# Kernel tuning notes

Hardware: AMD Instinct MI355X
Metric: run time of the kernel (lower is better)

The kernel has to match this reference:

```python
import jax, jax.numpy as jnp
import numpy as np

N_NODES = 80000
N_EDGES = 1280000
D_NODE = 128
D_EDGE = 32
D_HID = 64
NEG_SLOPE = 0.2


def setup_inputs() -> dict:
    key = jax.random.key(0)
    ks = jax.random.split(key, 9)
    return {
        "node_features": jax.random.normal(ks[0], (N_NODES, D_NODE), dtype=jnp.float32),
        "edge_features": jax.random.normal(ks[1], (N_EDGES, D_EDGE), dtype=jnp.float32),
        "edge_index": jax.random.randint(ks[2], (2, N_EDGES), 0, N_NODES, dtype=jnp.int64),
        # params: w (node Linear), edgew (edge Linear), attn (3*hid -> 1)
        "w_w": jax.random.normal(ks[3], (D_NODE, D_HID), dtype=jnp.float32) / np.sqrt(D_NODE),
        "w_b": jax.random.normal(ks[4], (D_HID,), dtype=jnp.float32) * 0.01,
        "ew_w": jax.random.normal(ks[5], (D_EDGE, D_HID), dtype=jnp.float32) / np.sqrt(D_EDGE),
        "ew_b": jax.random.normal(ks[6], (D_HID,), dtype=jnp.float32) * 0.01,
        "a_w": jax.random.normal(ks[7], (3 * D_HID, 1), dtype=jnp.float32) / np.sqrt(3 * D_HID),
        "a_b": jax.random.normal(ks[8], (1,), dtype=jnp.float32) * 0.01,
    }


def reference(node_features, edge_features, edge_index, w_w, w_b, ew_w, ew_b, a_w, a_b):
    n_nodes = node_features.shape[0]
    h = node_features @ w_w + w_b              # [N, H]
    edge_h = edge_features @ ew_w + ew_b       # [E, H]
    tgt = edge_index[0]                        # target (softmax group) nodes i
    nbr = edge_index[1]                        # neighbor nodes j
    h_i = h[tgt]                               # [E, H] gather
    h_j = h[nbr]                               # [E, H] gather
    h_concat = jnp.concatenate([h_i, h_j, edge_h], axis=-1)  # [E, 3H]
    eij = jax.nn.leaky_relu(h_concat @ a_w + a_b, negative_slope=NEG_SLOPE)  # [E, 1]
    # scatter-softmax over edges grouped by target node (numerically stable)
    seg_max = jax.ops.segment_max(eij, tgt, num_segments=n_nodes)            # [N, 1]
    ex = jnp.exp(eij - seg_max[tgt])
    seg_sum = jax.ops.segment_sum(ex, tgt, num_segments=n_nodes)             # [N, 1]
    alpha = ex / seg_sum[tgt]                                                # [E, 1]
    # (dropout omitted for deterministic reference)
    message = alpha * h_j                                                    # [E, H]
    out = jax.ops.segment_sum(message, tgt, num_segments=n_nodes)            # [N, H]
    return jax.nn.elu(out)
```

## Files before the change

kernel.cpp:

```cpp
#include <hip/hip_runtime.h>
#include <math.h>

#define N_NODES 80000
#define N_EDGES 1280000
#define D_NODE  128
#define D_EDGE  32
#define D_HID   64
#define NEG_SLOPE 0.2f
#define NB 313
#define CAP 4608
#define BCNT_STRIDE 16
#define EB_BLK 512
#define EB_CHUNK 2048
#define EB_NCHUNK (N_EDGES / EB_CHUNK)

__device__ inline float waveReduceSum(float v) {
    #pragma unroll
    for (int o = 32; o > 0; o >>= 1) v += __shfl_xor(v, o);
    return v;
}
__device__ inline unsigned short f2bf(float f) {
    unsigned u = __float_as_uint(f);
    return (unsigned short)((u + 0x7FFF + ((u >> 16) & 1)) >> 16);
}
__device__ inline float bf2f(unsigned short v) {
    return __uint_as_float(((unsigned)v) << 16);
}

__global__ __launch_bounds__(256) void node_kernel(
        const float* __restrict__ nf, const float* __restrict__ w_w,
        const float* __restrict__ w_b, const float* __restrict__ a_w,
        unsigned short* __restrict__ hb, float* __restrict__ s1, float* __restrict__ s2) {
    __shared__ float Ws[D_HID * D_NODE];
    __shared__ float Xs[32][D_NODE];
    for (int i = threadIdx.x; i < D_NODE * D_HID; i += 256) {
        int k = i >> 6, d = i & 63;
        Ws[d * D_NODE + (((k >> 2) ^ (d & 7)) << 2) + (k & 3)] = w_w[i];
    }
    int lane = threadIdx.x & 63;
    int wv   = threadIdx.x >> 6;
    float wb = w_b[lane];
    float a1 = a_w[lane];
    float a2 = a_w[D_HID + lane];
    const float* wrow = &Ws[lane * D_NODE];
    const int nTiles = N_NODES / 32;
    for (int tile = blockIdx.x; tile < nTiles; tile += gridDim.x) {
        int n0 = tile * 32;
        __syncthreads();
        {
            const float4* src = (const float4*)(nf + (size_t)n0 * D_NODE);
            float4* dst = (float4*)&Xs[0][0];
            #pragma unroll
            for (int j = 0; j < 4; ++j)
                dst[threadIdx.x + 256 * j] = src[threadIdx.x + 256 * j];
        }
        __syncthreads();
        float acc[8] = {0.f, 0.f, 0.f, 0.f, 0.f, 0.f, 0.f, 0.f};
        const float* xs = &Xs[wv * 8][0];
        #pragma unroll 4
        for (int k4 = 0; k4 < 32; ++k4) {
            float4 w = *(const float4*)&wrow[(k4 ^ (lane & 7)) << 2];
            #pragma unroll
            for (int n = 0; n < 8; ++n) {
                float4 x = *(const float4*)&xs[n * D_NODE + (k4 << 2)];
                acc[n] += w.x * x.x + w.y * x.y + w.z * x.z + w.w * x.w;
            }
        }
        #pragma unroll
        for (int n = 0; n < 8; ++n) {
            int node = n0 + wv * 8 + n;
            float hv = acc[n] + wb;
            hb[(size_t)node * D_HID + lane] = f2bf(hv);
            float r1 = waveReduceSum(hv * a1);
            float r2 = waveReduceSum(hv * a2);
            if (lane == 0) { s1[node] = r1; s2[node] = r2; }
        }
    }
}

__global__ __launch_bounds__(EB_BLK) void edge_bin_kernel(
        const float* __restrict__ ef, const int* __restrict__ eidx,
        const float* __restrict__ s2v,
        const float* __restrict__ ew_w, const float* __restrict__ ew_b,
        const float* __restrict__ a_w, const float* __restrict__ a_b,
        int* __restrict__ bcnt, int2* __restrict__ binned) {
    __shared__ float cs[D_EDGE];
    __shared__ float bes;
    __shared__ int hist[NB], gbase[NB], rank[NB];
    __shared__ int scanbuf[512];
    __shared__ float sq [EB_CHUNK];
    __shared__ int2  sval[EB_CHUNK];
    __shared__ int   sdst[EB_CHUNK];
    int tid = threadIdx.x;
    if (tid < D_EDGE) {
        float s = 0.f;
        #pragma unroll
        for (int d = 0; d < D_HID; ++d) s += ew_w[tid * D_HID + d] * a_w[2 * D_HID + d];
        cs[tid] = s;
    } else if (tid == D_EDGE) {
        float s = 0.f;
        #pragma unroll
        for (int d = 0; d < D_HID; ++d) s += ew_b[d] * a_w[2 * D_HID + d];
        bes = s + a_b[0];
    }
    int qd = tid >> 2;
    int j  = tid & 3;
    for (int c = blockIdx.x; c < EB_NCHUNK; c += gridDim.x) {
        for (int i = tid; i < NB; i += EB_BLK) { hist[i] = 0; rank[i] = 0; }
        __syncthreads();
        int e0 = c * EB_CHUNK;
        int RT[4], RN[4];
        #pragma unroll
        for (int k = 0; k < 4; ++k) {
            int idx = k * EB_BLK + tid;
            int e = e0 + idx;
            RT[k] = eidx[e];
            RN[k] = eidx[N_EDGES + e];
            sq[idx] = bes + s2v[RN[k]];
            atomicAdd(&hist[RT[k] >> 8], 1);
        }
        __syncthreads();
        #pragma unroll 2
        for (int rr = 0; rr < EB_CHUNK / 128; ++rr) {
            int idx = rr * 128 + qd;
            int e = e0 + idx;
            const float4* f4 = (const float4*)ef;
            float4 fa = f4[(size_t)e * 8 + j];
            float4 fb = f4[(size_t)e * 8 + 4 + j];
            const float4 c1 = *(const float4*)&cs[j * 4];
            const float4 c2 = *(const float4*)&cs[16 + j * 4];
            float p = fa.x * c1.x + fa.y * c1.y + fa.z * c1.z + fa.w * c1.w
                    + fb.x * c2.x + fb.y * c2.y + fb.z * c2.z + fb.w * c2.w;
            p += __shfl_xor(p, 1);
            p += __shfl_xor(p, 2);
            if (j == 0) sq[idx] += p;
        }
        __syncthreads();
        for (int i = tid; i < NB; i += EB_BLK) {
            int cc = hist[i];
            if (cc) gbase[i] = i * CAP + atomicAdd(&bcnt[i * BCNT_STRIDE], cc);
        }
        scanbuf[tid] = (tid < NB) ? hist[tid] : 0;
        __syncthreads();
        for (int ofs = 1; ofs < 512; ofs <<= 1) {
            int t = (tid >= (unsigned)ofs) ? scanbuf[tid - ofs] : 0;
            __syncthreads();
            scanbuf[tid] += t;
            __syncthreads();
        }
        #pragma unroll
        for (int k = 0; k < 4; ++k) {
            int idx = k * EB_BLK + tid;
            int tg = RT[k];
            int b  = tg >> 8;
            int r  = atomicAdd(&rank[b], 1);
            int slot = scanbuf[b] - hist[b] + r;
            sval[slot] = make_int2(((tg & 255) << 17) | RN[k],
                                   __float_as_int(sq[idx]));
            sdst[slot] = gbase[b] + r;
        }
        __syncthreads();
        #pragma unroll
        for (int k = 0; k < 4; ++k) {
            int i = k * EB_BLK + tid;
            binned[sdst[i]] = sval[i];
        }
        __syncthreads();
    }
}

__global__ __launch_bounds__(1024) void bucket_accum_kernel(
        const int* __restrict__ bcnt, const int2* __restrict__ binned,
        const float* __restrict__ s1, const unsigned short* __restrict__ hb,
        float* __restrict__ out) {
    __shared__ int nhist[256], buf[256], sbase[256], ncur[256];
    __shared__ int2 slab[CAP];
    int tid = threadIdx.x;
    int b = blockIdx.x;
    int in0 = b * CAP;
    int cnt = bcnt[b * BCNT_STRIDE];
    if (tid < 256) nhist[tid] = 0;
    __syncthreads();
    for (int i = tid; i < cnt; i += 1024)
        atomicAdd(&nhist[binned[in0 + i].x >> 17], 1);
    __syncthreads();
    if (tid < 256) buf[tid] = nhist[tid];
    __syncthreads();
    for (int ofs = 1; ofs < 256; ofs <<= 1) {
        int t = 0;
        if (tid < 256 && tid >= ofs) t = buf[tid - ofs];
        __syncthreads();
        if (tid < 256) buf[tid] += t;
        __syncthreads();
    }
    if (tid < 256) {
        int excl = buf[tid] - nhist[tid];
        sbase[tid] = excl;
        ncur[tid]  = excl;
    }
    __syncthreads();
    for (int i = tid; i < cnt; i += 1024) {
        int2 p = binned[in0 + i];
        int r = atomicAdd(&ncur[p.x >> 17], 1);
        slab[r] = make_int2(p.x & 0x1FFFF, p.y);
    }
    __syncthreads();
    int grp = tid >> 4;
    int li  = tid & 15;
    int wl  = ((tid & 63) >> 4) << 4;
    for (int nl = grp; nl < 256; nl += 64) {
        int node = b * 256 + nl;
        if (node >= N_NODES) break;
        int base = sbase[nl];
        int cn   = nhist[nl];
        float s1i = s1[node];
        float ax = 0.f, ay = 0.f, az = 0.f, aw = 0.f, sumex = 0.f;
        for (int c0 = 0; c0 < cn; c0 += 16) {
            int i = c0 + li;
            int nc = min(16, cn - c0);
            float exv = 0.f; int nbv = 0;
            if (i < cn) {
                int2 p = slab[base + i];
                nbv = p.x;
                float s = s1i + __int_as_float(p.y);
                s = (s > 0.f) ? s : NEG_SLOPE * s;
                exv = __expf(s);
            }
            sumex += exv;
            for (int jj = 0; jj < nc; ++jj) {
                float w  = __shfl(exv, wl + jj);
                int   nb = __shfl(nbv, wl + jj);
                uint2 v = *(const uint2*)&hb[(size_t)nb * D_HID + li * 4];
                ax += w * bf2f((unsigned short)(v.x & 0xFFFF));
                ay += w * bf2f((unsigned short)(v.x >> 16));
                az += w * bf2f((unsigned short)(v.y & 0xFFFF));
                aw += w * bf2f((unsigned short)(v.y >> 16));
            }
        }
        #pragma unroll
        for (int o = 8; o > 0; o >>= 1) sumex += __shfl_xor(sumex, o);
        float4 o4;
        if (cn == 0) {
            o4 = make_float4(0.f, 0.f, 0.f, 0.f);
        } else {
            o4.x = ax / sumex; o4.y = ay / sumex; o4.z = az / sumex; o4.w = aw / sumex;
            o4.x = (o4.x > 0.f) ? o4.x : (__expf(o4.x) - 1.f);
            o4.y = (o4.y > 0.f) ? o4.y : (__expf(o4.y) - 1.f);
            o4.z = (o4.z > 0.f) ? o4.z : (__expf(o4.z) - 1.f);
            o4.w = (o4.w > 0.f) ? o4.w : (__expf(o4.w) - 1.f);
        }
        ((float4*)out)[(size_t)node * 16 + li] = o4;
    }
}

extern "C" void kernel_launch(void* const* d_in, const int* in_sizes, int n_in,
                              void* d_out, int out_size, void* d_ws, size_t ws_size,
                              hipStream_t stream) {
    const float* nf   = (const float*)d_in[0];
    const float* ef   = (const float*)d_in[1];
    const int*   eidx = (const int*)d_in[2];
    const float* w_w  = (const float*)d_in[3];
    const float* w_b  = (const float*)d_in[4];
    const float* ew_w = (const float*)d_in[5];
    const float* ew_b = (const float*)d_in[6];
    const float* a_w  = (const float*)d_in[7];
    const float* a_b  = (const float*)d_in[8];
    float* out = (float*)d_out;

    char* ws = (char*)d_ws;
    size_t o = 0;
    auto alloc = [&](size_t bytes) -> void* {
        void* p = ws + o;
        o = (o + bytes + 255) & ~(size_t)255;
        return p;
    };
    unsigned short* hb  = (unsigned short*)alloc((size_t)N_NODES * D_HID * 2);
    float* s1       = (float*)alloc((size_t)N_NODES * 4);
    float* s2       = (float*)alloc((size_t)N_NODES * 4);
    int*   bcnt     = (int*)alloc((size_t)NB * BCNT_STRIDE * 4);
    int2*  binned   = (int2*)alloc((size_t)NB * CAP * 8);

    hipMemsetAsync(bcnt, 0, (size_t)NB * BCNT_STRIDE * 4, stream);

    node_kernel<<<1250, 256, 0, stream>>>(nf, w_w, w_b, a_w, hb, s1, s2);
    edge_bin_kernel<<<EB_NCHUNK, EB_BLK, 0, stream>>>(ef, eidx, s2, ew_w, ew_b, a_w, a_b, bcnt, binned);
    bucket_accum_kernel<<<NB, 1024, 0, stream>>>(bcnt, binned, s1, hb, out);
}
```

Measured before the change: 147.2 us.

## Fuse node projection and edge binning into one kernel; defer s2 gather

Merges the node linear kernel and the edge binning kernel into a single launch whose blocks are split by index into edge-binning blocks and node-projection blocks, so the two independent phases run concurrently. To remove the dependency of binning on the node scores, the per-neighbor s2 term is no longer gathered during binning and is instead gathered in the accumulation kernel. This trades one extra random gather per edge in the final kernel for overlap of the two phases and one fewer kernel launch. Node blocks now use 512 threads with 4 nodes per wave.

```diff
diff --git a/kernel.cpp b/kernel.cpp
--- a/kernel.cpp
+++ b/kernel.cpp
@@ -10,9 +10,10 @@
 #define NB 313
 #define CAP 4608
 #define BCNT_STRIDE 16
-#define EB_BLK 512
 #define EB_CHUNK 2048
-#define EB_NCHUNK (N_EDGES / EB_CHUNK)
+#define EB_NBLK 625
+#define ND_NBLK 1250
+#define ND_TILES 2500
 
 __device__ inline float waveReduceSum(float v) {
     #pragma unroll
@@ -27,116 +28,69 @@
     return __uint_as_float(((unsigned)v) << 16);
 }
 
-__global__ __launch_bounds__(256) void node_kernel(
-        const float* __restrict__ nf, const float* __restrict__ w_w,
-        const float* __restrict__ w_b, const float* __restrict__ a_w,
-        unsigned short* __restrict__ hb, float* __restrict__ s1, float* __restrict__ s2) {
-    __shared__ float Ws[D_HID * D_NODE];
-    __shared__ float Xs[32][D_NODE];
-    for (int i = threadIdx.x; i < D_NODE * D_HID; i += 256) {
-        int k = i >> 6, d = i & 63;
-        Ws[d * D_NODE + (((k >> 2) ^ (d & 7)) << 2) + (k & 3)] = w_w[i];
-    }
-    int lane = threadIdx.x & 63;
-    int wv   = threadIdx.x >> 6;
-    float wb = w_b[lane];
-    float a1 = a_w[lane];
-    float a2 = a_w[D_HID + lane];
-    const float* wrow = &Ws[lane * D_NODE];
-    const int nTiles = N_NODES / 32;
-    for (int tile = blockIdx.x; tile < nTiles; tile += gridDim.x) {
-        int n0 = tile * 32;
-        __syncthreads();
-        {
-            const float4* src = (const float4*)(nf + (size_t)n0 * D_NODE);
-            float4* dst = (float4*)&Xs[0][0];
-            #pragma unroll
-            for (int j = 0; j < 4; ++j)
-                dst[threadIdx.x + 256 * j] = src[threadIdx.x + 256 * j];
-        }
-        __syncthreads();
-        float acc[8] = {0.f, 0.f, 0.f, 0.f, 0.f, 0.f, 0.f, 0.f};
-        const float* xs = &Xs[wv * 8][0];
-        #pragma unroll 4
-        for (int k4 = 0; k4 < 32; ++k4) {
-            float4 w = *(const float4*)&wrow[(k4 ^ (lane & 7)) << 2];
-            #pragma unroll
-            for (int n = 0; n < 8; ++n) {
-                float4 x = *(const float4*)&xs[n * D_NODE + (k4 << 2)];
-                acc[n] += w.x * x.x + w.y * x.y + w.z * x.z + w.w * x.w;
-            }
-        }
-        #pragma unroll
-        for (int n = 0; n < 8; ++n) {
-            int node = n0 + wv * 8 + n;
-            float hv = acc[n] + wb;
-            hb[(size_t)node * D_HID + lane] = f2bf(hv);
-            float r1 = waveReduceSum(hv * a1);
-            float r2 = waveReduceSum(hv * a2);
-            if (lane == 0) { s1[node] = r1; s2[node] = r2; }
-        }
-    }
-}
-
-__global__ __launch_bounds__(EB_BLK) void edge_bin_kernel(
-        const float* __restrict__ ef, const int* __restrict__ eidx,
-        const float* __restrict__ s2v,
+__global__ __launch_bounds__(512) void fused_kernel(
+        const float* __restrict__ nf, const float* __restrict__ ef,
+        const int* __restrict__ eidx,
+        const float* __restrict__ w_w, const float* __restrict__ w_b,
         const float* __restrict__ ew_w, const float* __restrict__ ew_b,
         const float* __restrict__ a_w, const float* __restrict__ a_b,
+        unsigned short* __restrict__ hb, float* __restrict__ s1, float* __restrict__ s2,
         int* __restrict__ bcnt, int2* __restrict__ binned) {
-    __shared__ float cs[D_EDGE];
-    __shared__ float bes;
-    __shared__ int hist[NB], gbase[NB], rank[NB];
-    __shared__ int scanbuf[512];
-    __shared__ float sq [EB_CHUNK];
-    __shared__ int2  sval[EB_CHUNK];
-    __shared__ int   sdst[EB_CHUNK];
+    __shared__ __align__(16) char smem[49152];
     int tid = threadIdx.x;
-    if (tid < D_EDGE) {
-        float s = 0.f;
-        #pragma unroll
-        for (int d = 0; d < D_HID; ++d) s += ew_w[tid * D_HID + d] * a_w[2 * D_HID + d];
-        cs[tid] = s;
-    } else if (tid == D_EDGE) {
-        float s = 0.f;
-        #pragma unroll
-        for (int d = 0; d < D_HID; ++d) s += ew_b[d] * a_w[2 * D_HID + d];
-        bes = s + a_b[0];
-    }
-    int qd = tid >> 2;
-    int j  = tid & 3;
-    for (int c = blockIdx.x; c < EB_NCHUNK; c += gridDim.x) {
-        for (int i = tid; i < NB; i += EB_BLK) { hist[i] = 0; rank[i] = 0; }
-        __syncthreads();
-        int e0 = c * EB_CHUNK;
+
+    if (blockIdx.x < EB_NBLK) {
+        float* cs      = (float*)smem;
+        float* besp    = (float*)(smem + 128);
+        int*   hist    = (int*)(smem + 256);
+        int*   gbase   = (int*)(smem + 1536);
+        int*   rank    = (int*)(smem + 2816);
+        int*   scanbuf = (int*)(smem + 4096);
+        float* sq      = (float*)(smem + 6144);
+        int2*  sval    = (int2*)(smem + 14336);
+        int*   sdst    = (int*)(smem + 30720);
+        if (tid < D_EDGE) {
+            float s = 0.f;
+            #pragma unroll
+            for (int d = 0; d < D_HID; ++d) s += ew_w[tid * D_HID + d] * a_w[2 * D_HID + d];
+            cs[tid] = s;
+        } else if (tid == D_EDGE) {
+            float s = 0.f;
+            #pragma unroll
+            for (int d = 0; d < D_HID; ++d) s += ew_b[d] * a_w[2 * D_HID + d];
+            *besp = s + a_b[0];
+        }
+        for (int i = tid; i < NB; i += 512) { hist[i] = 0; rank[i] = 0; }
+        __syncthreads();
+        float bes = *besp;
+        int e0 = blockIdx.x * EB_CHUNK;
         int RT[4], RN[4];
         #pragma unroll
         for (int k = 0; k < 4; ++k) {
-            int idx = k * EB_BLK + tid;
+            int idx = k * 512 + tid;
             int e = e0 + idx;
             RT[k] = eidx[e];
             RN[k] = eidx[N_EDGES + e];
-            sq[idx] = bes + s2v[RN[k]];
             atomicAdd(&hist[RT[k] >> 8], 1);
         }
-        __syncthreads();
+        int qd = tid >> 2, j = tid & 3;
+        const float4 c1 = *(const float4*)&cs[j * 4];
+        const float4 c2 = *(const float4*)&cs[16 + j * 4];
+        const float4* f4 = (const float4*)ef;
         #pragma unroll 2
         for (int rr = 0; rr < EB_CHUNK / 128; ++rr) {
             int idx = rr * 128 + qd;
             int e = e0 + idx;
-            const float4* f4 = (const float4*)ef;
             float4 fa = f4[(size_t)e * 8 + j];
             float4 fb = f4[(size_t)e * 8 + 4 + j];
-            const float4 c1 = *(const float4*)&cs[j * 4];
-            const float4 c2 = *(const float4*)&cs[16 + j * 4];
             float p = fa.x * c1.x + fa.y * c1.y + fa.z * c1.z + fa.w * c1.w
                     + fb.x * c2.x + fb.y * c2.y + fb.z * c2.z + fb.w * c2.w;
             p += __shfl_xor(p, 1);
             p += __shfl_xor(p, 2);
-            if (j == 0) sq[idx] += p;
-        }
-        __syncthreads();
-        for (int i = tid; i < NB; i += EB_BLK) {
+            if (j == 0) sq[idx] = p + bes;
+        }
+        __syncthreads();
+        for (int i = tid; i < NB; i += 512) {
             int cc = hist[i];
             if (cc) gbase[i] = i * CAP + atomicAdd(&bcnt[i * BCNT_STRIDE], cc);
         }
@@ -150,7 +104,7 @@
         }
         #pragma unroll
         for (int k = 0; k < 4; ++k) {
-            int idx = k * EB_BLK + tid;
+            int idx = k * 512 + tid;
             int tg = RT[k];
             int b  = tg >> 8;
             int r  = atomicAdd(&rank[b], 1);
@@ -162,17 +116,60 @@
         __syncthreads();
         #pragma unroll
         for (int k = 0; k < 4; ++k) {
-            int i = k * EB_BLK + tid;
+            int i = k * 512 + tid;
             binned[sdst[i]] = sval[i];
         }
-        __syncthreads();
+    } else {
+        float* Ws = (float*)smem;
+        float* Xs = (float*)(smem + 32768);
+        for (int i = tid; i < D_NODE * D_HID; i += 512) {
+            int k = i >> 6, d = i & 63;
+            Ws[d * D_NODE + (((k >> 2) ^ (d & 7)) << 2) + (k & 3)] = w_w[i];
+        }
+        int lane = tid & 63;
+        int wv   = tid >> 6;
+        float wb = w_b[lane];
+        float a1 = a_w[lane];
+        float a2 = a_w[D_HID + lane];
+        const float* wrow = &Ws[lane * D_NODE];
+        for (int tile = (int)blockIdx.x - EB_NBLK; tile < ND_TILES; tile += ND_NBLK) {
+            int n0 = tile * 32;
+            __syncthreads();
+            {
+                const float4* src = (const float4*)(nf + (size_t)n0 * D_NODE);
+                float4* dst = (float4*)Xs;
+                dst[tid]       = src[tid];
+                dst[tid + 512] = src[tid + 512];
+            }
+            __syncthreads();
+            float acc[4] = {0.f, 0.f, 0.f, 0.f};
+            const float* xs = &Xs[(size_t)wv * 4 * D_NODE];
+            #pragma unroll 4
+            for (int k4 = 0; k4 < 32; ++k4) {
+                float4 w = *(const float4*)&wrow[(k4 ^ (lane & 7)) << 2];
+                #pragma unroll
+                for (int n = 0; n < 4; ++n) {
+                    float4 x = *(const float4*)&xs[n * D_NODE + (k4 << 2)];
+                    acc[n] += w.x * x.x + w.y * x.y + w.z * x.z + w.w * x.w;
+                }
+            }
+            #pragma unroll
+            for (int n = 0; n < 4; ++n) {
+                int node = n0 + wv * 4 + n;
+                float hv = acc[n] + wb;
+                hb[(size_t)node * D_HID + lane] = f2bf(hv);
+                float r1 = waveReduceSum(hv * a1);
+                float r2 = waveReduceSum(hv * a2);
+                if (lane == 0) { s1[node] = r1; s2[node] = r2; }
+            }
+        }
     }
 }
 
 __global__ __launch_bounds__(1024) void bucket_accum_kernel(
         const int* __restrict__ bcnt, const int2* __restrict__ binned,
-        const float* __restrict__ s1, const unsigned short* __restrict__ hb,
-        float* __restrict__ out) {
+        const float* __restrict__ s1, const float* __restrict__ s2v,
+        const unsigned short* __restrict__ hb, float* __restrict__ out) {
     __shared__ int nhist[256], buf[256], sbase[256], ncur[256];
     __shared__ int2 slab[CAP];
     int tid = threadIdx.x;
@@ -222,7 +219,7 @@
             if (i < cn) {
                 int2 p = slab[base + i];
                 nbv = p.x;
-                float s = s1i + __int_as_float(p.y);
+                float s = s1i + __int_as_float(p.y) + s2v[nbv];
                 s = (s > 0.f) ? s : NEG_SLOPE * s;
                 exv = __expf(s);
             }
@@ -282,7 +279,7 @@
 
     hipMemsetAsync(bcnt, 0, (size_t)NB * BCNT_STRIDE * 4, stream);
 
-    node_kernel<<<1250, 256, 0, stream>>>(nf, w_w, w_b, a_w, hb, s1, s2);
-    edge_bin_kernel<<<EB_NCHUNK, EB_BLK, 0, stream>>>(ef, eidx, s2, ew_w, ew_b, a_w, a_b, bcnt, binned);
-    bucket_accum_kernel<<<NB, 1024, 0, stream>>>(bcnt, binned, s1, hb, out);
-}
+    fused_kernel<<<EB_NBLK + ND_NBLK, 512, 0, stream>>>(
+        nf, ef, eidx, w_w, w_b, ew_w, ew_b, a_w, a_b, hb, s1, s2, bcnt, binned);
+    bucket_accum_kernel<<<NB, 1024, 0, stream>>>(bcnt, binned, s1, s2, hb, out);
+}
```

Result: no change. 147.8 us (+0.4%).

## Move s2 gather into accumulate kernel and batch edge-feature loads for MLP

Applied to the files above, without the earlier changes.

Drops the per-edge random gather of s2[nbr] from the binning kernel and instead adds s2 inside the bucket accumulate kernel, where the neighbor index is already at hand. The edge-feature dot product now issues eight float4 loads per half before computing, to raise memory-level parallelism. The grid-stride loop is removed since the grid equals the chunk count. This decouples the binning kernel from the node kernel's s2 output, at the cost of an extra scattered 4-byte load per edge in the accumulate phase.

```diff
diff --git a/kernel.cpp b/kernel.cpp
--- a/kernel.cpp
+++ b/kernel.cpp
@@ -80,12 +80,11 @@
 
 __global__ __launch_bounds__(EB_BLK) void edge_bin_kernel(
         const float* __restrict__ ef, const int* __restrict__ eidx,
-        const float* __restrict__ s2v,
         const float* __restrict__ ew_w, const float* __restrict__ ew_b,
         const float* __restrict__ a_w, const float* __restrict__ a_b,
         int* __restrict__ bcnt, int2* __restrict__ binned) {
     __shared__ float cs[D_EDGE];
-    __shared__ float bes;
+    __shared__ float besp;
     __shared__ int hist[NB], gbase[NB], rank[NB];
     __shared__ int scanbuf[512];
     __shared__ float sq [EB_CHUNK];
@@ -101,78 +100,83 @@
         float s = 0.f;
         #pragma unroll
         for (int d = 0; d < D_HID; ++d) s += ew_b[d] * a_w[2 * D_HID + d];
-        bes = s + a_b[0];
-    }
-    int qd = tid >> 2;
-    int j  = tid & 3;
-    for (int c = blockIdx.x; c < EB_NCHUNK; c += gridDim.x) {
-        for (int i = tid; i < NB; i += EB_BLK) { hist[i] = 0; rank[i] = 0; }
-        __syncthreads();
-        int e0 = c * EB_CHUNK;
-        int RT[4], RN[4];
-        #pragma unroll
-        for (int k = 0; k < 4; ++k) {
-            int idx = k * EB_BLK + tid;
-            int e = e0 + idx;
-            RT[k] = eidx[e];
-            RN[k] = eidx[N_EDGES + e];
-            sq[idx] = bes + s2v[RN[k]];
-            atomicAdd(&hist[RT[k] >> 8], 1);
-        }
-        __syncthreads();
-        #pragma unroll 2
-        for (int rr = 0; rr < EB_CHUNK / 128; ++rr) {
-            int idx = rr * 128 + qd;
-            int e = e0 + idx;
-            const float4* f4 = (const float4*)ef;
-            float4 fa = f4[(size_t)e * 8 + j];
-            float4 fb = f4[(size_t)e * 8 + 4 + j];
-            const float4 c1 = *(const float4*)&cs[j * 4];
-            const float4 c2 = *(const float4*)&cs[16 + j * 4];
-            float p = fa.x * c1.x + fa.y * c1.y + fa.z * c1.z + fa.w * c1.w
-                    + fb.x * c2.x + fb.y * c2.y + fb.z * c2.z + fb.w * c2.w;
-            p += __shfl_xor(p, 1);
-            p += __shfl_xor(p, 2);
-            if (j == 0) sq[idx] += p;
-        }
-        __syncthreads();
-        for (int i = tid; i < NB; i += EB_BLK) {
-            int cc = hist[i];
-            if (cc) gbase[i] = i * CAP + atomicAdd(&bcnt[i * BCNT_STRIDE], cc);
-        }
-        scanbuf[tid] = (tid < NB) ? hist[tid] : 0;
-        __syncthreads();
-        for (int ofs = 1; ofs < 512; ofs <<= 1) {
-            int t = (tid >= (unsigned)ofs) ? scanbuf[tid - ofs] : 0;
-            __syncthreads();
-            scanbuf[tid] += t;
-            __syncthreads();
-        }
-        #pragma unroll
-        for (int k = 0; k < 4; ++k) {
-            int idx = k * EB_BLK + tid;
-            int tg = RT[k];
-            int b  = tg >> 8;
-            int r  = atomicAdd(&rank[b], 1);
-            int slot = scanbuf[b] - hist[b] + r;
-            sval[slot] = make_int2(((tg & 255) << 17) | RN[k],
-                                   __float_as_int(sq[idx]));
-            sdst[slot] = gbase[b] + r;
-        }
-        __syncthreads();
-        #pragma unroll
-        for (int k = 0; k < 4; ++k) {
-            int i = k * EB_BLK + tid;
-            binned[sdst[i]] = sval[i];
-        }
-        __syncthreads();
+        besp = s + a_b[0];
+    }
+    for (int i = tid; i < NB; i += EB_BLK) { hist[i] = 0; rank[i] = 0; }
+    __syncthreads();
+    float bes = besp;
+    int e0 = blockIdx.x * EB_CHUNK;
+    int RT[4], RN[4];
+    #pragma unroll
+    for (int k = 0; k < 4; ++k) {
+        int idx = k * EB_BLK + tid;
+        int e = e0 + idx;
+        RT[k] = eidx[e];
+        RN[k] = eidx[N_EDGES + e];
+        atomicAdd(&hist[RT[k] >> 8], 1);
+    }
+    {
+        int qd = tid >> 2, j = tid & 3;
+        const float4 c1 = *(const float4*)&cs[j * 4];
+        const float4 c2 = *(const float4*)&cs[16 + j * 4];
+        const float4* f4 = (const float4*)ef;
+        #pragma unroll
+        for (int half = 0; half < 2; ++half) {
+            float4 FA[8], FB[8];
+            #pragma unroll
+            for (int rr = 0; rr < 8; ++rr) {
+                int idx = (half * 8 + rr) * 128 + qd;
+                size_t e = (size_t)(e0 + idx);
+                FA[rr] = f4[e * 8 + j];
+                FB[rr] = f4[e * 8 + 4 + j];
+            }
+            #pragma unroll
+            for (int rr = 0; rr < 8; ++rr) {
+                int idx = (half * 8 + rr) * 128 + qd;
+                float p = FA[rr].x * c1.x + FA[rr].y * c1.y + FA[rr].z * c1.z + FA[rr].w * c1.w
+                        + FB[rr].x * c2.x + FB[rr].y * c2.y + FB[rr].z * c2.z + FB[rr].w * c2.w;
+                p += __shfl_xor(p, 1);
+                p += __shfl_xor(p, 2);
+                if (j == 0) sq[idx] = p + bes;
+            }
+        }
+    }
+    __syncthreads();
+    for (int i = tid; i < NB; i += EB_BLK) {
+        int cc = hist[i];
+        if (cc) gbase[i] = i * CAP + atomicAdd(&bcnt[i * BCNT_STRIDE], cc);
+    }
+    scanbuf[tid] = (tid < NB) ? hist[tid] : 0;
+    __syncthreads();
+    for (int ofs = 1; ofs < 512; ofs <<= 1) {
+        int t = (tid >= (unsigned)ofs) ? scanbuf[tid - ofs] : 0;
+        __syncthreads();
+        scanbuf[tid] += t;
+        __syncthreads();
+    }
+    #pragma unroll
+    for (int k = 0; k < 4; ++k) {
+        int idx = k * EB_BLK + tid;
+        int tg = RT[k];
+        int b  = tg >> 8;
+        int r  = atomicAdd(&rank[b], 1);
+        int slot = scanbuf[b] - hist[b] + r;
+        sval[slot] = make_int2(((tg & 255) << 17) | RN[k],
+                               __float_as_int(sq[idx]));
+        sdst[slot] = gbase[b] + r;
+    }
+    __syncthreads();
+    #pragma unroll
+    for (int k = 0; k < 4; ++k) {
+        int i = k * EB_BLK + tid;
+        binned[sdst[i]] = sval[i];
     }
 }
 
 __global__ __launch_bounds__(1024) void bucket_accum_kernel(
         const int* __restrict__ bcnt, const int2* __restrict__ binned,
-        const float* __restrict__ s1, const unsigned short* __restrict__ hb,
-        float* __restrict__ out) {
+        const float* __restrict__ s1, const float* __restrict__ s2v,
+        const unsigned short* __restrict__ hb, float* __restrict__ out) {
     __shared__ int nhist[256], buf[256], sbase[256], ncur[256];
     __shared__ int2 slab[CAP];
     int tid = threadIdx.x;
@@ -222,7 +226,7 @@
             if (i < cn) {
                 int2 p = slab[base + i];
                 nbv = p.x;
-                float s = s1i + __int_as_float(p.y);
+                float s = s1i + __int_as_float(p.y) + s2v[nbv];
                 s = (s > 0.f) ? s : NEG_SLOPE * s;
                 exv = __expf(s);
             }
@@ -283,6 +287,6 @@
     hipMemsetAsync(bcnt, 0, (size_t)NB * BCNT_STRIDE * 4, stream);
 
     node_kernel<<<1250, 256, 0, stream>>>(nf, w_w, w_b, a_w, hb, s1, s2);
-    edge_bin_kernel<<<EB_NCHUNK, EB_BLK, 0, stream>>>(ef, eidx, s2, ew_w, ew_b, a_w, a_b, bcnt, binned);
-    bucket_accum_kernel<<<NB, 1024, 0, stream>>>(bcnt, binned, s1, hb, out);
-}
+    edge_bin_kernel<<<EB_NCHUNK, EB_BLK, 0, stream>>>(ef, eidx, ew_w, ew_b, a_w, a_b, bcnt, binned);
+    bucket_accum_kernel<<<NB, 1024, 0, stream>>>(bcnt, binned, s1, s2, hb, out);
+}
```

Result: slower. 150.7 us (+2.4%).
